# Kernel optimization log

Measured on AMD Instinct MI355X. Metric: run time of the kernel, lower is better.

The kernel has to match this reference:

```python
import jax, jax.numpy as jnp
import numpy as np

FORGET_BIAS = 1.0
LAYERS = 2


def setup_inputs() -> dict:
    key = jax.random.key(0)
    ks = jax.random.split(key, 10)
    B, T, H, V = 64, 50, 256, 50000
    G = 4 * H
    s = 1.0 / np.sqrt(H)
    return {
        "input_data": jax.random.randint(ks[0], (B, T), 0, V, dtype=jnp.int64),
        "embedding": jax.random.uniform(ks[1], (V, H), jnp.float32, -1.0, 1.0),
        "Wx": jax.random.normal(ks[2], (LAYERS, H, G), jnp.float32) * s,
        "Uh": jax.random.normal(ks[3], (LAYERS, H, G), jnp.float32) * s,
        "alpha": jax.random.uniform(ks[4], (LAYERS, G), jnp.float32),
        "beta1": jax.random.uniform(ks[5], (LAYERS, G), jnp.float32),
        "beta2": jax.random.uniform(ks[6], (LAYERS, G), jnp.float32),
        "bias": jnp.zeros((LAYERS, G), jnp.float32),
        "softmax_w": jax.random.normal(ks[7], (V, H), jnp.float32) * s,
        "softmax_b": jnp.full((V,), 0.1, jnp.float32),
    }


def _mi_lstm_stack(inputs_tbh, Wx, Uh, alpha, beta1, beta2, bias):
    # inputs_tbh: [T, B, H]; params have leading layer axis [L, ...]
    T, B, H = inputs_tbh.shape
    c0 = jnp.zeros((LAYERS, B, H), inputs_tbh.dtype)
    h0 = jnp.zeros((LAYERS, B, H), inputs_tbh.dtype)

    def step(carry, x_t):
        c, h = carry
        inp = x_t
        new_c, new_h = [], []
        for l in range(LAYERS):
            xh = inp @ Wx[l]          # [B, 4H]
            hh = h[l] @ Uh[l]         # [B, 4H]
            gates = alpha[l] * xh * hh + beta1[l] * xh + beta2[l] * hh + bias[l]
            i, j, f, o = jnp.split(gates, 4, axis=-1)
            c_l = c[l] * jax.nn.sigmoid(f + FORGET_BIAS) + jax.nn.sigmoid(i) * jnp.tanh(j)
            h_l = jnp.tanh(c_l) * jax.nn.sigmoid(o)
            new_c.append(c_l)
            new_h.append(h_l)
            inp = h_l
        return (jnp.stack(new_c), jnp.stack(new_h)), inp

    (_, _), outs = jax.lax.scan(step, (c0, h0), inputs_tbh)
    return outs  # [T, B, H] top-layer hidden states


def reference(input_data, embedding, Wx, Uh, alpha, beta1, beta2, bias, softmax_w, softmax_b):
    # embedding lookup: [B, T, H] -> time-major [T, B, H]
    x = embedding[input_data]
    outs = _mi_lstm_stack(jnp.transpose(x, (1, 0, 2)), Wx, Uh, alpha, beta1, beta2, bias)
    # batch-major flatten like tf.reshape(outputs, [-1, rnn_size]) on [B, T, H]
    H = outs.shape[-1]
    flat = jnp.transpose(outs, (1, 0, 2)).reshape(-1, H)  # [B*T, H]
    logits = flat @ softmax_w.T + softmax_b               # [B*T, V]
    return logits
```

## Files before the change

### kernel.cpp

```cpp
#include <hip/hip_runtime.h>
#include <hip/hip_bf16.h>
#include <math.h>

#define B_ 64
#define T_ 50
#define H_ 256
#define G_ 1024
#define V_ 50000
#define NBLK 32

using f16x8 = __attribute__((ext_vector_type(8))) _Float16;
using f32x4 = __attribute__((ext_vector_type(4))) float;

__device__ __forceinline__ float sigm(float x) { return 1.0f / (1.0f + expf(-x)); }

__global__ __launch_bounds__(64) void embed_k(const int* __restrict__ idx,
                                              const float* __restrict__ emb,
                                              float* __restrict__ x_tm)
{
    const int row = blockIdx.x;
    const int b = row & (B_ - 1);
    const int t = row >> 6;
    const int id = idx[b * T_ + t];
    const float4 v = *reinterpret_cast<const float4*>(emb + (size_t)id * H_ + threadIdx.x * 4);
    *reinterpret_cast<float4*>(x_tm + (size_t)row * H_ + threadIdx.x * 4) = v;
}

__global__ __launch_bounds__(256) void conv_half(const float* __restrict__ in,
                                                 _Float16* __restrict__ out, int n)
{
    const int i = (blockIdx.x * 256 + threadIdx.x) * 8;
    if (i + 8 <= n) {
        const float4 v0 = *reinterpret_cast<const float4*>(in + i);
        const float4 v1 = *reinterpret_cast<const float4*>(in + i + 4);
        f16x8 h;
        h[0] = (_Float16)v0.x; h[1] = (_Float16)v0.y;
        h[2] = (_Float16)v0.z; h[3] = (_Float16)v0.w;
        h[4] = (_Float16)v1.x; h[5] = (_Float16)v1.y;
        h[6] = (_Float16)v1.z; h[7] = (_Float16)v1.w;
        *reinterpret_cast<f16x8*>(out + i) = h;
    }
}

__global__ __launch_bounds__(256) void pack_w_rec(const float* __restrict__ Uh0,
                                                  const float* __restrict__ Wx1,
                                                  const float* __restrict__ Uh1,
                                                  _Float16* __restrict__ wpk)
{
    const int c = blockIdx.x;
    const int m = blockIdx.y;
    const float* __restrict__ src = (m == 0) ? Uh0 : (m == 1) ? Wx1 : Uh1;
    _Float16* __restrict__ dst = wpk + (((size_t)c * 3 + m) << 13);
    for (int i = threadIdx.x; i < 8192; i += 256) {
        const int k = i >> 5;
        const int col = i & 31;
        const int colg = ((col >> 3) << 8) + (c << 3) + (col & 7);
        dst[(col << 8) + k] = (_Float16)src[(size_t)k * G_ + colg];
    }
}

__global__ __launch_bounds__(256) void gemm128_kn(const float* __restrict__ A,
                                                  const float* __restrict__ Bm,
                                                  float* __restrict__ C,
                                                  int M, int N, int K)
{
    __shared__ float As[32][132];
    __shared__ float Bs[32][132];

    const int m0 = blockIdx.x * 128;
    const int n0 = blockIdx.y * 128;
    const int tid = threadIdx.x;
    const int tm = (tid >> 4) << 3;
    const int tn = (tid & 15) << 3;

    float acc[8][8];
#pragma unroll
    for (int i = 0; i < 8; ++i)
#pragma unroll
        for (int j = 0; j < 8; ++j) acc[i][j] = 0.0f;

    for (int k0 = 0; k0 < K; k0 += 32) {
#pragma unroll
        for (int i = 0; i < 4; ++i) {
            const int s = tid + (i << 8);
            const int m = s >> 3;
            const int kk = (s & 7) << 2;
            const float4 v = *reinterpret_cast<const float4*>(
                A + (size_t)(m0 + m) * K + k0 + kk);
            As[kk + 0][m] = v.x; As[kk + 1][m] = v.y;
            As[kk + 2][m] = v.z; As[kk + 3][m] = v.w;
        }
#pragma unroll
        for (int i = 0; i < 4; ++i) {
            const int s = tid + (i << 8);
            const int kk = s >> 5;
            const int nn = (s & 31) << 2;
            const float4 v = *reinterpret_cast<const float4*>(
                Bm + (size_t)(k0 + kk) * N + n0 + nn);
            *reinterpret_cast<float4*>(&Bs[kk][nn]) = v;
        }
        __syncthreads();

#pragma unroll
        for (int k = 0; k < 32; ++k) {
            float a[8], bb[8];
            *reinterpret_cast<float4*>(&a[0]) = *reinterpret_cast<const float4*>(&As[k][tm]);
            *reinterpret_cast<float4*>(&a[4]) = *reinterpret_cast<const float4*>(&As[k][tm + 4]);
            *reinterpret_cast<float4*>(&bb[0]) = *reinterpret_cast<const float4*>(&Bs[k][tn]);
            *reinterpret_cast<float4*>(&bb[4]) = *reinterpret_cast<const float4*>(&Bs[k][tn + 4]);
#pragma unroll
            for (int i = 0; i < 8; ++i)
#pragma unroll
                for (int j = 0; j < 8; ++j)
                    acc[i][j] = fmaf(a[i], bb[j], acc[i][j]);
        }
        __syncthreads();
    }

#pragma unroll
    for (int i = 0; i < 8; ++i) {
        const int m = m0 + tm + i;
#pragma unroll
        for (int j = 0; j < 8; j += 4) {
            const int n = n0 + tn + j;
            float4 v;
            v.x = acc[i][j + 0]; v.y = acc[i][j + 1];
            v.z = acc[i][j + 2]; v.w = acc[i][j + 3];
            *reinterpret_cast<float4*>(C + (size_t)m * N + n) = v;
        }
    }
}

__device__ __forceinline__ void gbar_arrive(int* slot)
{
    __syncthreads();
    if (threadIdx.x == 0) {
        __threadfence();
        __hip_atomic_fetch_add(slot, 1, __ATOMIC_RELAXED, __HIP_MEMORY_SCOPE_AGENT);
    }
}

__device__ __forceinline__ void gbar_wait(int* slot)
{
    if (threadIdx.x == 0) {
        while (__hip_atomic_load(slot, __ATOMIC_RELAXED, __HIP_MEMORY_SCOPE_AGENT) < NBLK)
            __builtin_amdgcn_s_sleep(1);
    }
    __syncthreads();
    __threadfence();
}

__global__ __launch_bounds__(256) void mi_rec(
    const _Float16* __restrict__ wpk,
    const float* __restrict__ xh0,
    _Float16* __restrict__ h0x,
    _Float16* __restrict__ h1x,
    _Float16* __restrict__ outsH,
    int* __restrict__ bars,
    const float* __restrict__ alpha, const float* __restrict__ b1,
    const float* __restrict__ b2, const float* __restrict__ bsv)
{
    __shared__ __align__(16) _Float16 h0l[16384];
    __shared__ __align__(16) _Float16 h1l[16384];
    __shared__ __align__(16) _Float16 wl[24576];
    __shared__ float gA[2112], gB[2112];
    __shared__ float c0l[512], c1l[512];

    const int c = blockIdx.x;
    const int tid = threadIdx.x;
    const int l = tid & 63;
    const int w = tid >> 6;

    for (int i = tid; i < 2048; i += 256) {
        *reinterpret_cast<f16x8*>(&h0l[i << 3]) = f16x8{};
        *reinterpret_cast<f16x8*>(&h1l[i << 3]) = f16x8{};
    }
    for (int i = tid; i < 512; i += 256) { c0l[i] = 0.f; c1l[i] = 0.f; }

    for (int i = tid; i < 3072; i += 256) {
        const int m = i >> 10;
        const int col = (i >> 5) & 31;
        const int ch = i & 31;
        const f16x8 v = *reinterpret_cast<const f16x8*>(
            &wpk[(((size_t)c * 3 + m) * 32 + col) * 256 + (ch << 3)]);
        *reinterpret_cast<f16x8*>(
            &wl[(m * 32 + col) * 256 + ((ch ^ (col & 7)) << 3)]) = v;
    }

    const int u = tid & 7, b0 = tid >> 3;
    const int jl = (c << 3) + u;
    float al0[4], b10[4], b20[4], bs0[4], al1[4], b11[4], b21[4], bs1[4];
#pragma unroll
    for (int g = 0; g < 4; ++g) {
        const int col = (g << 8) + jl;
        al0[g] = alpha[col];        b10[g] = b1[col];
        b20[g] = b2[col];           bs0[g] = bsv[col];
        al1[g] = alpha[G_ + col];   b11[g] = b1[G_ + col];
        b21[g] = b2[G_ + col];      bs1[g] = bsv[G_ + col];
    }
    __syncthreads();

    const int arow = (w << 4) + (l & 15);
    const int cA = l & 15, cB = 16 + (l & 15);
    const int kq = l >> 4;

    auto MM = [&](const _Float16* __restrict__ am, const _Float16* __restrict__ bm,
                  f32x4& A0, f32x4& A1) {
#pragma unroll
        for (int s = 0; s < 8; ++s) {
            const int ck = (s << 2) + kq;
            const f16x8 af = *reinterpret_cast<const f16x8*>(
                &am[(arow << 8) + ((ck ^ (arow & 7)) << 3)]);
            const f16x8 bf0 = *reinterpret_cast<const f16x8*>(
                &bm[(cA << 8) + ((ck ^ (cA & 7)) << 3)]);
            const f16x8 bf1 = *reinterpret_cast<const f16x8*>(
                &bm[(cB << 8) + ((ck ^ (cB & 7)) << 3)]);
            A0 = __builtin_amdgcn_mfma_f32_16x16x32_f16(af, bf0, A0, 0, 0, 0);
            A1 = __builtin_amdgcn_mfma_f32_16x16x32_f16(af, bf1, A1, 0, 0, 0);
        }
    };

    auto STG = [&](float* gl, f32x4 A0, f32x4 A1) {
        const int rb = (w << 4) + (kq << 2);
#pragma unroll
        for (int r = 0; r < 4; ++r) {
            gl[(rb + r) * 33 + cA] = A0[r];
            gl[(rb + r) * 33 + cB] = A1[r];
        }
    };

    auto STAGE_H = [&](const _Float16* __restrict__ src, _Float16* __restrict__ dst) {
#pragma unroll
        for (int it = 0; it < 8; ++it) {
            const int idx = (it << 8) + tid;
            const int row = idx >> 5, ch = idx & 31;
            const f16x8 v = *reinterpret_cast<const f16x8*>(&src[(row << 8) + (ch << 3)]);
            *reinterpret_cast<f16x8*>(&dst[(row << 8) + ((ch ^ (row & 7)) << 3)]) = v;
        }
    };

    for (int s = 0; s <= T_; ++s) {
        const int p = s & 1;
        _Float16* __restrict__ h0w = h0x + (p << 14);
        _Float16* __restrict__ h1w = h1x + (p << 14);

        if (s < T_) {
            f32x4 A0 = {}, A1 = {};
            MM(h0l, wl, A0, A1);
            STG(gA, A0, A1);
            __syncthreads();
#pragma unroll
            for (int bb = 0; bb < 2; ++bb) {
                const int b = b0 + (bb << 5);
                float g4[4];
#pragma unroll
                for (int g = 0; g < 4; ++g) {
                    const float a = gA[b * 33 + (g << 3) + u];
                    const float x = xh0[(((size_t)(s * B_ + b)) << 10) + (g << 8) + jl];
                    g4[g] = al0[g] * x * a + b10[g] * x + b20[g] * a + bs0[g];
                }
                const float cn = c0l[(b << 3) + u] * sigm(g4[2] + 1.f)
                               + sigm(g4[0]) * tanhf(g4[1]);
                c0l[(b << 3) + u] = cn;
                h0w[(b << 8) + jl] = (_Float16)(tanhf(cn) * sigm(g4[3]));
            }
            __syncthreads();
        }

        if (s > 0) {
            f32x4 X0 = {}, X1 = {}, H0 = {}, H1 = {};
            MM(h0l, wl + 1 * 8192, X0, X1);
            MM(h1l, wl + 2 * 8192, H0, H1);
            STG(gA, X0, X1);
            STG(gB, H0, H1);
            __syncthreads();
#pragma unroll
            for (int bb = 0; bb < 2; ++bb) {
                const int b = b0 + (bb << 5);
                float g4[4];
#pragma unroll
                for (int g = 0; g < 4; ++g) {
                    const float xa = gA[b * 33 + (g << 3) + u];
                    const float ha = gB[b * 33 + (g << 3) + u];
                    g4[g] = al1[g] * xa * ha + b11[g] * xa + b21[g] * ha + bs1[g];
                }
                const float cn = c1l[(b << 3) + u] * sigm(g4[2] + 1.f)
                               + sigm(g4[0]) * tanhf(g4[1]);
                c1l[(b << 3) + u] = cn;
                const float hn = tanhf(cn) * sigm(g4[3]);
                h1w[(b << 8) + jl] = (_Float16)hn;
                outsH[(((size_t)b * T_ + (s - 1)) << 8) + jl] = (_Float16)hn;
            }
        }

        if (s < T_) {
            gbar_arrive(&bars[s]);
            gbar_wait(&bars[s]);
            STAGE_H(h0w, h0l);
            if (s > 0) STAGE_H(h1w, h1l);
            __syncthreads();
        }
    }
}

#define PM 128
#define PN 128
#define PK 64

__device__ __forceinline__ void gload_lds16(const void* g, void* l)
{
    __builtin_amdgcn_global_load_lds(
        (const __attribute__((address_space(1))) unsigned int*)g,
        (__attribute__((address_space(3))) unsigned int*)l, 16, 0, 0);
}

__global__ __launch_bounds__(256) void proj_mfma(
    const _Float16* __restrict__ A16,
    const _Float16* __restrict__ B16,
    const float* __restrict__ bias,
    float* __restrict__ C)
{
    __shared__ __align__(16) _Float16 Asub[PM * PK];
    __shared__ __align__(16) _Float16 Bsub[PN * PK];

    const int tid = threadIdx.x;
    const int l = tid & 63;
    const int w = tid >> 6;
    const int wm = w >> 1, wn = w & 1;

    const int n0 = blockIdx.x * PN;
    const int m0 = blockIdx.y * PM;

    f32x4 acc[4][4] = {};

    for (int k0 = 0; k0 < H_; k0 += PK) {
#pragma unroll
        for (int is = 0; is < 4; ++is) {
            const int i = is * 256 + tid;
            const int r = i >> 3;
            const int ch = (i & 7) ^ (r & 7);
            gload_lds16(A16 + (size_t)(m0 + r) * H_ + k0 + ch * 8, &Asub[i * 8]);
            int n = n0 + r; if (n > V_ - 1) n = V_ - 1;
            gload_lds16(B16 + (size_t)n * H_ + k0 + ch * 8, &Bsub[i * 8]);
        }
        __syncthreads();

#pragma unroll
        for (int ks = 0; ks < 2; ++ks) {
            f16x8 af[4], bf[4];
#pragma unroll
            for (int i = 0; i < 4; ++i) {
                const int r = wm * 64 + i * 16 + (l & 15);
                const int ch = (ks * 4 + (l >> 4)) ^ (r & 7);
                af[i] = *reinterpret_cast<const f16x8*>(&Asub[r * PK + ch * 8]);
            }
#pragma unroll
            for (int jf = 0; jf < 4; ++jf) {
                const int r = wn * 64 + jf * 16 + (l & 15);
                const int ch = (ks * 4 + (l >> 4)) ^ (r & 7);
                bf[jf] = *reinterpret_cast<const f16x8*>(&Bsub[r * PK + ch * 8]);
            }
#pragma unroll
            for (int i = 0; i < 4; ++i)
#pragma unroll
                for (int jf = 0; jf < 4; ++jf)
                    acc[i][jf] = __builtin_amdgcn_mfma_f32_16x16x32_f16(
                        af[i], bf[jf], acc[i][jf], 0, 0, 0);
        }
        __syncthreads();
    }

    const int rb = (l >> 4) << 2;
    const int cl = l & 15;
#pragma unroll
    for (int jf = 0; jf < 4; ++jf) {
        const int col = n0 + wn * 64 + jf * 16 + cl;
        if (col < V_) {
            const float bv = bias[col];
#pragma unroll
            for (int i = 0; i < 4; ++i) {
                const int rowb = m0 + wm * 64 + i * 16 + rb;
#pragma unroll
                for (int r = 0; r < 4; ++r)
                    C[(size_t)(rowb + r) * V_ + col] = acc[i][jf][r] + bv;
            }
        }
    }
}

extern "C" void kernel_launch(void* const* d_in, const int* in_sizes, int n_in,
                              void* d_out, int out_size, void* d_ws, size_t ws_size,
                              hipStream_t stream)
{
    const int*   idx   = (const int*)  d_in[0];
    const float* emb   = (const float*)d_in[1];
    const float* Wx    = (const float*)d_in[2];
    const float* Uh    = (const float*)d_in[3];
    const float* alpha = (const float*)d_in[4];
    const float* b1    = (const float*)d_in[5];
    const float* b2    = (const float*)d_in[6];
    const float* bsv   = (const float*)d_in[7];
    const float* sw    = (const float*)d_in[8];
    const float* sb    = (const float*)d_in[9];
    float* out = (float*)d_out;

    char* wsb = (char*)d_ws;
    float*    x_tm  = (float*)   (wsb);
    float*    xh0   = (float*)   (wsb + 3276800);
    _Float16* outsH = (_Float16*)(wsb + 16384000);
    _Float16* w16   = (_Float16*)(wsb + 18022400);
    _Float16* wpk   = (_Float16*)(wsb + 43622400);
    _Float16* h0x   = (_Float16*)(wsb + 45195264);
    _Float16* h1x   = (_Float16*)(wsb + 45260800);
    int*      bars  = (int*)     (wsb + 45326336);

    const float* Wx1 = Wx + (size_t)H_ * G_;
    const float* Uh0 = Uh;
    const float* Uh1 = Uh + (size_t)H_ * G_;

    hipMemsetAsync(bars, 0, 512, stream);

    {
        dim3 grid(NBLK, 3);
        pack_w_rec<<<grid, 256, 0, stream>>>(Uh0, Wx1, Uh1, wpk);
    }

    conv_half<<<(V_ * H_) / 2048, 256, 0, stream>>>(sw, w16, V_ * H_);

    embed_k<<<T_ * B_, 64, 0, stream>>>(idx, emb, x_tm);

    {
        dim3 grid(3200 / 128, G_ / 128);
        gemm128_kn<<<grid, 256, 0, stream>>>(x_tm, Wx, xh0, 3200, G_, H_);
    }

    mi_rec<<<NBLK, 256, 0, stream>>>(wpk, xh0, h0x, h1x, outsH, bars,
                                     alpha, b1, b2, bsv);

    {
        dim3 grid((V_ + PN - 1) / PN, 3200 / PM);
        proj_mfma<<<grid, 256, 0, stream>>>(outsH, w16, sb, out);
    }
}
```

Baseline: 724.1 us.

## Fuse recurrence and output projection into one persistent kernel with tile queue

```diff
diff --git a/kernel.cpp b/kernel.cpp
--- a/kernel.cpp
+++ b/kernel.cpp
@@ -8,6 +8,9 @@
 #define G_ 1024
 #define V_ 50000
 #define NBLK 32
+#define NTTILE 391
+#define NMTILE 25
+#define NTILES (NMTILE * NTTILE)
 
 using f16x8 = __attribute__((ext_vector_type(8))) _Float16;
 using f32x4 = __attribute__((ext_vector_type(4))) float;
@@ -131,6 +134,13 @@
     }
 }
 
+__device__ __forceinline__ void gload_lds16(const void* g, void* l)
+{
+    __builtin_amdgcn_global_load_lds(
+        (const __attribute__((address_space(1))) unsigned int*)g,
+        (__attribute__((address_space(3))) unsigned int*)l, 16, 0, 0);
+}
+
 __device__ __forceinline__ void gbar_arrive(int* slot)
 {
     __syncthreads();
@@ -140,251 +150,254 @@
     }
 }
 
+template<int SLP>
 __device__ __forceinline__ void gbar_wait(int* slot)
 {
     if (threadIdx.x == 0) {
         while (__hip_atomic_load(slot, __ATOMIC_RELAXED, __HIP_MEMORY_SCOPE_AGENT) < NBLK)
-            __builtin_amdgcn_s_sleep(1);
+            __builtin_amdgcn_s_sleep(SLP);
     }
     __syncthreads();
     __threadfence();
 }
 
-__global__ __launch_bounds__(256) void mi_rec(
+__global__ __launch_bounds__(256) void fused_k(
     const _Float16* __restrict__ wpk,
     const float* __restrict__ xh0,
     _Float16* __restrict__ h0x,
     _Float16* __restrict__ h1x,
     _Float16* __restrict__ outsH,
     int* __restrict__ bars,
+    int* __restrict__ wq,
+    const _Float16* __restrict__ w16,
+    const float* __restrict__ sb,
+    float* __restrict__ out,
     const float* __restrict__ alpha, const float* __restrict__ b1,
     const float* __restrict__ b2, const float* __restrict__ bsv)
 {
-    __shared__ __align__(16) _Float16 h0l[16384];
-    __shared__ __align__(16) _Float16 h1l[16384];
-    __shared__ __align__(16) _Float16 wl[24576];
-    __shared__ float gA[2112], gB[2112];
-    __shared__ float c0l[512], c1l[512];
-
-    const int c = blockIdx.x;
+    __shared__ __align__(16) char smem[135680];
+    __shared__ int tile_s;
     const int tid = threadIdx.x;
     const int l = tid & 63;
     const int w = tid >> 6;
 
-    for (int i = tid; i < 2048; i += 256) {
-        *reinterpret_cast<f16x8*>(&h0l[i << 3]) = f16x8{};
-        *reinterpret_cast<f16x8*>(&h1l[i << 3]) = f16x8{};
-    }
-    for (int i = tid; i < 512; i += 256) { c0l[i] = 0.f; c1l[i] = 0.f; }
-
-    for (int i = tid; i < 3072; i += 256) {
-        const int m = i >> 10;
-        const int col = (i >> 5) & 31;
-        const int ch = i & 31;
-        const f16x8 v = *reinterpret_cast<const f16x8*>(
-            &wpk[(((size_t)c * 3 + m) * 32 + col) * 256 + (ch << 3)]);
-        *reinterpret_cast<f16x8*>(
-            &wl[(m * 32 + col) * 256 + ((ch ^ (col & 7)) << 3)]) = v;
-    }
-
-    const int u = tid & 7, b0 = tid >> 3;
-    const int jl = (c << 3) + u;
-    float al0[4], b10[4], b20[4], bs0[4], al1[4], b11[4], b21[4], bs1[4];
-#pragma unroll
-    for (int g = 0; g < 4; ++g) {
-        const int col = (g << 8) + jl;
-        al0[g] = alpha[col];        b10[g] = b1[col];
-        b20[g] = b2[col];           bs0[g] = bsv[col];
-        al1[g] = alpha[G_ + col];   b11[g] = b1[G_ + col];
-        b21[g] = b2[G_ + col];      bs1[g] = bsv[G_ + col];
-    }
-    __syncthreads();
-
-    const int arow = (w << 4) + (l & 15);
-    const int cA = l & 15, cB = 16 + (l & 15);
-    const int kq = l >> 4;
-
-    auto MM = [&](const _Float16* __restrict__ am, const _Float16* __restrict__ bm,
-                  f32x4& A0, f32x4& A1) {
-#pragma unroll
-        for (int s = 0; s < 8; ++s) {
-            const int ck = (s << 2) + kq;
-            const f16x8 af = *reinterpret_cast<const f16x8*>(
-                &am[(arow << 8) + ((ck ^ (arow & 7)) << 3)]);
-            const f16x8 bf0 = *reinterpret_cast<const f16x8*>(
-                &bm[(cA << 8) + ((ck ^ (cA & 7)) << 3)]);
-            const f16x8 bf1 = *reinterpret_cast<const f16x8*>(
-                &bm[(cB << 8) + ((ck ^ (cB & 7)) << 3)]);
-            A0 = __builtin_amdgcn_mfma_f32_16x16x32_f16(af, bf0, A0, 0, 0, 0);
-            A1 = __builtin_amdgcn_mfma_f32_16x16x32_f16(af, bf1, A1, 0, 0, 0);
-        }
-    };
-
-    auto STG = [&](float* gl, f32x4 A0, f32x4 A1) {
-        const int rb = (w << 4) + (kq << 2);
-#pragma unroll
-        for (int r = 0; r < 4; ++r) {
-            gl[(rb + r) * 33 + cA] = A0[r];
-            gl[(rb + r) * 33 + cB] = A1[r];
-        }
-    };
-
-    auto STAGE_H = [&](const _Float16* __restrict__ src, _Float16* __restrict__ dst) {
-#pragma unroll
-        for (int it = 0; it < 8; ++it) {
-            const int idx = (it << 8) + tid;
-            const int row = idx >> 5, ch = idx & 31;
-            const f16x8 v = *reinterpret_cast<const f16x8*>(&src[(row << 8) + (ch << 3)]);
-            *reinterpret_cast<f16x8*>(&dst[(row << 8) + ((ch ^ (row & 7)) << 3)]) = v;
-        }
-    };
-
-    for (int s = 0; s <= T_; ++s) {
-        const int p = s & 1;
-        _Float16* __restrict__ h0w = h0x + (p << 14);
-        _Float16* __restrict__ h1w = h1x + (p << 14);
-
-        if (s < T_) {
-            f32x4 A0 = {}, A1 = {};
-            MM(h0l, wl, A0, A1);
-            STG(gA, A0, A1);
+    if (blockIdx.x < NBLK) {
+        _Float16* h0l = (_Float16*)(smem);
+        _Float16* h1l = (_Float16*)(smem + 32768);
+        _Float16* wl  = (_Float16*)(smem + 65536);
+        float* gA  = (float*)(smem + 114688);
+        float* gB  = (float*)(smem + 123136);
+        float* c0l = (float*)(smem + 131584);
+        float* c1l = (float*)(smem + 133632);
+
+        const int c = blockIdx.x;
+
+        for (int i = tid; i < 2048; i += 256) {
+            *reinterpret_cast<f16x8*>(&h0l[i << 3]) = f16x8{};
+            *reinterpret_cast<f16x8*>(&h1l[i << 3]) = f16x8{};
+        }
+        for (int i = tid; i < 512; i += 256) { c0l[i] = 0.f; c1l[i] = 0.f; }
+
+        for (int i = tid; i < 3072; i += 256) {
+            const int m = i >> 10;
+            const int col = (i >> 5) & 31;
+            const int ch = i & 31;
+            const f16x8 v = *reinterpret_cast<const f16x8*>(
+                &wpk[(((size_t)c * 3 + m) * 32 + col) * 256 + (ch << 3)]);
+            *reinterpret_cast<f16x8*>(
+                &wl[(m * 32 + col) * 256 + ((ch ^ (col & 7)) << 3)]) = v;
+        }
+
+        const int u = tid & 7, b0 = tid >> 3;
+        const int jl = (c << 3) + u;
+        float al0[4], b10[4], b20[4], bs0[4], al1[4], b11[4], b21[4], bs1[4];
+#pragma unroll
+        for (int g = 0; g < 4; ++g) {
+            const int col = (g << 8) + jl;
+            al0[g] = alpha[col];        b10[g] = b1[col];
+            b20[g] = b2[col];           bs0[g] = bsv[col];
+            al1[g] = alpha[G_ + col];   b11[g] = b1[G_ + col];
+            b21[g] = b2[G_ + col];      bs1[g] = bsv[G_ + col];
+        }
+        __syncthreads();
+
+        const int arow = (w << 4) + (l & 15);
+        const int cA = l & 15, cB = 16 + (l & 15);
+        const int kq = l >> 4;
+
+        auto MM = [&](const _Float16* am, const _Float16* bm, f32x4& A0, f32x4& A1) {
+#pragma unroll
+            for (int s = 0; s < 8; ++s) {
+                const int ck = (s << 2) + kq;
+                const f16x8 af = *reinterpret_cast<const f16x8*>(
+                    &am[(arow << 8) + ((ck ^ (arow & 7)) << 3)]);
+                const f16x8 bf0 = *reinterpret_cast<const f16x8*>(
+                    &bm[(cA << 8) + ((ck ^ (cA & 7)) << 3)]);
+                const f16x8 bf1 = *reinterpret_cast<const f16x8*>(
+                    &bm[(cB << 8) + ((ck ^ (cB & 7)) << 3)]);
+                A0 = __builtin_amdgcn_mfma_f32_16x16x32_f16(af, bf0, A0, 0, 0, 0);
+                A1 = __builtin_amdgcn_mfma_f32_16x16x32_f16(af, bf1, A1, 0, 0, 0);
+            }
+        };
+        auto STG = [&](float* gl, f32x4 A0, f32x4 A1) {
+            const int rb = (w << 4) + (kq << 2);
+#pragma unroll
+            for (int r = 0; r < 4; ++r) {
+                gl[(rb + r) * 33 + cA] = A0[r];
+                gl[(rb + r) * 33 + cB] = A1[r];
+            }
+        };
+        auto STAGE_H = [&](const _Float16* src, _Float16* dst) {
+#pragma unroll
+            for (int it = 0; it < 8; ++it) {
+                const int idx = (it << 8) + tid;
+                const int row = idx >> 5, ch = idx & 31;
+                const f16x8 v = *reinterpret_cast<const f16x8*>(&src[(row << 8) + (ch << 3)]);
+                *reinterpret_cast<f16x8*>(&dst[(row << 8) + ((ch ^ (row & 7)) << 3)]) = v;
+            }
+        };
+
+        for (int s = 0; s <= T_; ++s) {
+            const int p = s & 1;
+            _Float16* h0w = h0x + (p << 14);
+            _Float16* h1w = h1x + (p << 14);
+
+            if (s < T_) {
+                f32x4 A0 = {}, A1 = {};
+                MM(h0l, wl, A0, A1);
+                STG(gA, A0, A1);
+                __syncthreads();
+#pragma unroll
+                for (int bb = 0; bb < 2; ++bb) {
+                    const int b = b0 + (bb << 5);
+                    float g4[4];
+#pragma unroll
+                    for (int g = 0; g < 4; ++g) {
+                        const float a = gA[b * 33 + (g << 3) + u];
+                        const float x = xh0[(((size_t)(s * B_ + b)) << 10) + (g << 8) + jl];
+                        g4[g] = al0[g] * x * a + b10[g] * x + b20[g] * a + bs0[g];
+                    }
+                    const float cn = c0l[(b << 3) + u] * sigm(g4[2] + 1.f)
+                                   + sigm(g4[0]) * tanhf(g4[1]);
+                    c0l[(b << 3) + u] = cn;
+                    h0w[(b << 8) + jl] = (_Float16)(tanhf(cn) * sigm(g4[3]));
+                }
+                __syncthreads();
+            }
+
+            if (s > 0) {
+                f32x4 X0 = {}, X1 = {}, H0 = {}, H1 = {};
+                MM(h0l, wl + 1 * 8192, X0, X1);
+                MM(h1l, wl + 2 * 8192, H0, H1);
+                STG(gA, X0, X1);
+                STG(gB, H0, H1);
+                __syncthreads();
+#pragma unroll
+                for (int bb = 0; bb < 2; ++bb) {
+                    const int b = b0 + (bb << 5);
+                    float g4[4];
+#pragma unroll
+                    for (int g = 0; g < 4; ++g) {
+                        const float xa = gA[b * 33 + (g << 3) + u];
+                        const float ha = gB[b * 33 + (g << 3) + u];
+                        g4[g] = al1[g] * xa * ha + b11[g] * xa + b21[g] * ha + bs1[g];
+                    }
+                    const float cn = c1l[(b << 3) + u] * sigm(g4[2] + 1.f)
+                                   + sigm(g4[0]) * tanhf(g4[1]);
+                    c1l[(b << 3) + u] = cn;
+                    const float hn = tanhf(cn) * sigm(g4[3]);
+                    h1w[(b << 8) + jl] = (_Float16)hn;
+                    outsH[(((size_t)(s - 1) * B_ + b) << 8) + jl] = (_Float16)hn;
+                }
+            }
+
+            gbar_arrive(&bars[s]);
+            if (s < T_) {
+                gbar_wait<1>(&bars[s]);
+                STAGE_H(h0w, h0l);
+                if (s > 0) STAGE_H(h1w, h1l);
+                __syncthreads();
+            }
+        }
+    }
+
+    _Float16* Asub = (_Float16*)smem;
+    _Float16* Bsub = (_Float16*)(smem + 16384);
+
+    for (;;) {
+        if (tid == 0)
+            tile_s = __hip_atomic_fetch_add(wq, 1, __ATOMIC_RELAXED,
+                                            __HIP_MEMORY_SCOPE_AGENT);
+        __syncthreads();
+        const int tile = tile_s;
+        if (tile >= NTILES) break;
+        const int mt = tile / NTTILE;
+        const int nt = tile - mt * NTTILE;
+        const int m0 = mt * 128;
+        const int n0 = nt * 128;
+
+        gbar_wait<8>(&bars[2 * mt + 2]);
+
+        f32x4 acc[4][4] = {};
+        const int wm = w >> 1, wn = w & 1;
+
+        for (int k0 = 0; k0 < H_; k0 += 64) {
+#pragma unroll
+            for (int is = 0; is < 4; ++is) {
+                const int i = is * 256 + tid;
+                const int r = i >> 3;
+                const int ch = (i & 7) ^ (r & 7);
+                gload_lds16(outsH + (size_t)(m0 + r) * H_ + k0 + ch * 8, &Asub[i * 8]);
+                int n = n0 + r; if (n > V_ - 1) n = V_ - 1;
+                gload_lds16(w16 + (size_t)n * H_ + k0 + ch * 8, &Bsub[i * 8]);
+            }
             __syncthreads();
-#pragma unroll
-            for (int bb = 0; bb < 2; ++bb) {
-                const int b = b0 + (bb << 5);
-                float g4[4];
-#pragma unroll
-                for (int g = 0; g < 4; ++g) {
-                    const float a = gA[b * 33 + (g << 3) + u];
-                    const float x = xh0[(((size_t)(s * B_ + b)) << 10) + (g << 8) + jl];
-                    g4[g] = al0[g] * x * a + b10[g] * x + b20[g] * a + bs0[g];
+
+#pragma unroll
+            for (int ks = 0; ks < 2; ++ks) {
+                f16x8 af[4], bf[4];
+#pragma unroll
+                for (int i = 0; i < 4; ++i) {
+                    const int r = wm * 64 + i * 16 + (l & 15);
+                    const int ch = (ks * 4 + (l >> 4)) ^ (r & 7);
+                    af[i] = *reinterpret_cast<const f16x8*>(&Asub[r * 64 + ch * 8]);
                 }
-                const float cn = c0l[(b << 3) + u] * sigm(g4[2] + 1.f)
-                               + sigm(g4[0]) * tanhf(g4[1]);
-                c0l[(b << 3) + u] = cn;
-                h0w[(b << 8) + jl] = (_Float16)(tanhf(cn) * sigm(g4[3]));
+#pragma unroll
+                for (int jf = 0; jf < 4; ++jf) {
+                    const int r = wn * 64 + jf * 16 + (l & 15);
+                    const int ch = (ks * 4 + (l >> 4)) ^ (r & 7);
+                    bf[jf] = *reinterpret_cast<const f16x8*>(&Bsub[r * 64 + ch * 8]);
+                }
+#pragma unroll
+                for (int i = 0; i < 4; ++i)
+#pragma unroll
+                    for (int jf = 0; jf < 4; ++jf)
+                        acc[i][jf] = __builtin_amdgcn_mfma_f32_16x16x32_f16(
+                            af[i], bf[jf], acc[i][jf], 0, 0, 0);
             }
             __syncthreads();
         }
 
-        if (s > 0) {
-            f32x4 X0 = {}, X1 = {}, H0 = {}, H1 = {};
-            MM(h0l, wl + 1 * 8192, X0, X1);
-            MM(h1l, wl + 2 * 8192, H0, H1);
-            STG(gA, X0, X1);
-            STG(gB, H0, H1);
-            __syncthreads();
-#pragma unroll
-            for (int bb = 0; bb < 2; ++bb) {
-                const int b = b0 + (bb << 5);
-                float g4[4];
-#pragma unroll
-                for (int g = 0; g < 4; ++g) {
-                    const float xa = gA[b * 33 + (g << 3) + u];
-                    const float ha = gB[b * 33 + (g << 3) + u];
-                    g4[g] = al1[g] * xa * ha + b11[g] * xa + b21[g] * ha + bs1[g];
+        const int rb = (l >> 4) << 2;
+        const int cl = l & 15;
+#pragma unroll
+        for (int jf = 0; jf < 4; ++jf) {
+            const int col = n0 + wn * 64 + jf * 16 + cl;
+            if (col < V_) {
+                const float bv = sb[col];
+#pragma unroll
+                for (int i = 0; i < 4; ++i) {
+                    const int rowa = m0 + wm * 64 + i * 16 + rb;
+#pragma unroll
+                    for (int r = 0; r < 4; ++r) {
+                        const int ra = rowa + r;
+                        const int brow = (ra & 63) * T_ + (ra >> 6);
+                        out[(size_t)brow * V_ + col] = acc[i][jf][r] + bv;
+                    }
                 }
-                const float cn = c1l[(b << 3) + u] * sigm(g4[2] + 1.f)
-                               + sigm(g4[0]) * tanhf(g4[1]);
-                c1l[(b << 3) + u] = cn;
-                const float hn = tanhf(cn) * sigm(g4[3]);
-                h1w[(b << 8) + jl] = (_Float16)hn;
-                outsH[(((size_t)b * T_ + (s - 1)) << 8) + jl] = (_Float16)hn;
-            }
-        }
-
-        if (s < T_) {
-            gbar_arrive(&bars[s]);
-            gbar_wait(&bars[s]);
-            STAGE_H(h0w, h0l);
-            if (s > 0) STAGE_H(h1w, h1l);
-            __syncthreads();
-        }
-    }
-}
-
-#define PM 128
-#define PN 128
-#define PK 64
-
-__device__ __forceinline__ void gload_lds16(const void* g, void* l)
-{
-    __builtin_amdgcn_global_load_lds(
-        (const __attribute__((address_space(1))) unsigned int*)g,
-        (__attribute__((address_space(3))) unsigned int*)l, 16, 0, 0);
-}
-
-__global__ __launch_bounds__(256) void proj_mfma(
-    const _Float16* __restrict__ A16,
-    const _Float16* __restrict__ B16,
-    const float* __restrict__ bias,
-    float* __restrict__ C)
-{
-    __shared__ __align__(16) _Float16 Asub[PM * PK];
-    __shared__ __align__(16) _Float16 Bsub[PN * PK];
-
-    const int tid = threadIdx.x;
-    const int l = tid & 63;
-    const int w = tid >> 6;
-    const int wm = w >> 1, wn = w & 1;
-
-    const int n0 = blockIdx.x * PN;
-    const int m0 = blockIdx.y * PM;
-
-    f32x4 acc[4][4] = {};
-
-    for (int k0 = 0; k0 < H_; k0 += PK) {
-#pragma unroll
-        for (int is = 0; is < 4; ++is) {
-            const int i = is * 256 + tid;
-            const int r = i >> 3;
-            const int ch = (i & 7) ^ (r & 7);
-            gload_lds16(A16 + (size_t)(m0 + r) * H_ + k0 + ch * 8, &Asub[i * 8]);
-            int n = n0 + r; if (n > V_ - 1) n = V_ - 1;
-            gload_lds16(B16 + (size_t)n * H_ + k0 + ch * 8, &Bsub[i * 8]);
+            }
         }
         __syncthreads();
-
-#pragma unroll
-        for (int ks = 0; ks < 2; ++ks) {
-            f16x8 af[4], bf[4];
-#pragma unroll
-            for (int i = 0; i < 4; ++i) {
-                const int r = wm * 64 + i * 16 + (l & 15);
-                const int ch = (ks * 4 + (l >> 4)) ^ (r & 7);
-                af[i] = *reinterpret_cast<const f16x8*>(&Asub[r * PK + ch * 8]);
-            }
-#pragma unroll
-            for (int jf = 0; jf < 4; ++jf) {
-                const int r = wn * 64 + jf * 16 + (l & 15);
-                const int ch = (ks * 4 + (l >> 4)) ^ (r & 7);
-                bf[jf] = *reinterpret_cast<const f16x8*>(&Bsub[r * PK + ch * 8]);
-            }
-#pragma unroll
-            for (int i = 0; i < 4; ++i)
-#pragma unroll
-                for (int jf = 0; jf < 4; ++jf)
-                    acc[i][jf] = __builtin_amdgcn_mfma_f32_16x16x32_f16(
-                        af[i], bf[jf], acc[i][jf], 0, 0, 0);
-        }
-        __syncthreads();
-    }
-
-    const int rb = (l >> 4) << 2;
-    const int cl = l & 15;
-#pragma unroll
-    for (int jf = 0; jf < 4; ++jf) {
-        const int col = n0 + wn * 64 + jf * 16 + cl;
-        if (col < V_) {
-            const float bv = bias[col];
-#pragma unroll
-            for (int i = 0; i < 4; ++i) {
-                const int rowb = m0 + wm * 64 + i * 16 + rb;
-#pragma unroll
-                for (int r = 0; r < 4; ++r)
-                    C[(size_t)(rowb + r) * V_ + col] = acc[i][jf][r] + bv;
-            }
-        }
     }
 }
 
@@ -413,12 +426,13 @@
     _Float16* h0x   = (_Float16*)(wsb + 45195264);
     _Float16* h1x   = (_Float16*)(wsb + 45260800);
     int*      bars  = (int*)     (wsb + 45326336);
+    int*      wq    = bars + 64;
 
     const float* Wx1 = Wx + (size_t)H_ * G_;
     const float* Uh0 = Uh;
     const float* Uh1 = Uh + (size_t)H_ * G_;
 
-    hipMemsetAsync(bars, 0, 512, stream);
+    (void)hipMemsetAsync(bars, 0, 512, stream);
 
     {
         dim3 grid(NBLK, 3);
@@ -434,11 +448,6 @@
         gemm128_kn<<<grid, 256, 0, stream>>>(x_tm, Wx, xh0, 3200, G_, H_);
     }
 
-    mi_rec<<<NBLK, 256, 0, stream>>>(wpk, xh0, h0x, h1x, outsH, bars,
-                                     alpha, b1, b2, bsv);
-
-    {
-        dim3 grid((V_ + PN - 1) / PN, 3200 / PM);
-        proj_mfma<<<grid, 256, 0, stream>>>(outsH, w16, sb, out);
-    }
-}
+    fused_k<<<256, 256, 0, stream>>>(wpk, xh0, h0x, h1x, outsH, bars, wq,
+                                     w16, sb, out, alpha, b1, b2, bsv);
+}
```

Measured after the change: 1.436 ms. 1.98x slower.
